# Performance work log

Measured on AMD Instinct MI355X. Metric: run time of the kernel, lower is better.

Reference implementation:

```python
import jax, jax.numpy as jnp
import numpy as np

TOP_K_FRACTION = 0.1


def setup_inputs() -> dict:
    key = jax.random.key(0)
    k1, k2, k3 = jax.random.split(key, 3)
    B, H, S, D = 2, 12, 1024, 64
    q = jax.random.normal(k1, (B, H, S, D), dtype=jnp.float32)
    k = jax.random.normal(k2, (B, H, S, D), dtype=jnp.float32)
    v = jax.random.normal(k3, (B, H, S, D), dtype=jnp.float32)
    mask = jnp.zeros((B, 1, 1, S), dtype=jnp.float32)
    return {"q": q, "k": k, "v": v, "mask": mask}


def reference(q, k, v, mask):
    B, H, S, D = q.shape
    k_precise = max(1, int(S * TOP_K_FRACTION))
    # binary (sign) approximation of attention scores; detached like torch
    q_bin = jnp.sign(jax.lax.stop_gradient(q))
    k_bin = jnp.sign(jax.lax.stop_gradient(k))
    approx_scores = jnp.einsum('bhsd,bhtd->bhst', q_bin, k_bin) / D  # [B,H,S,S]
    _, topk_idx = jax.lax.top_k(approx_scores, k_precise)  # [B,H,S,kp]
    # gather top-k keys/values per query: [B,H,S,kp,D]
    k_gathered = jnp.take_along_axis(k[:, :, None, :, :], topk_idx[..., None], axis=3)
    v_gathered = jnp.take_along_axis(v[:, :, None, :, :], topk_idx[..., None], axis=3)
    scale = np.float32(1.0 / np.sqrt(D))
    precise_scores = jnp.einsum('bhsd,bhskd->bhsk', q, k_gathered) * scale
    # gather mask along key positions: mask [B,1,1,S] -> [B,H,S,kp]
    mask_gathered = jnp.take_along_axis(
        jnp.broadcast_to(mask, (B, H, S, S)), topk_idx, axis=-1)
    precise_scores = precise_scores + mask_gathered
    precise_probs = jax.nn.softmax(precise_scores, axis=-1)
    attn_output = jnp.einsum('bhsk,bhskd->bhsd', precise_probs, v_gathered)
    return attn_output
```

## Files before the change

kernel.cpp:

```cpp
#include <hip/hip_runtime.h>
#include <hip/hip_fp16.h>
#include <cstdint>

#define BB 2
#define HH 12
#define SS 1024
#define DD 64
#define KP 102
#define KPAD 104
#define QPB 4
#define PFD 4

typedef _Float16 half2v __attribute__((ext_vector_type(2)));
typedef _Float16 half8v __attribute__((ext_vector_type(8)));
typedef float    f32x4  __attribute__((ext_vector_type(4)));

template <int CTRL>
__device__ __forceinline__ float dpp_f(float x) {
    return __builtin_bit_cast(float,
        __builtin_amdgcn_update_dpp(0, __builtin_bit_cast(int, x), CTRL, 0xF, 0xF, false));
}
__device__ __forceinline__ float group8_sum(float x) {
    x += dpp_f<0xB1>(x);
    x += dpp_f<0x4E>(x);
    x += dpp_f<0x141>(x);
    return x;
}
__device__ __forceinline__ int mbcnt64(unsigned long long m) {
    return (int)__builtin_amdgcn_mbcnt_hi((unsigned)(m >> 32),
               __builtin_amdgcn_mbcnt_lo((unsigned)(m & 0xffffffffull), 0u));
}
__device__ __forceinline__ half2v shfl_xor_h2(half2v v, int m) {
    return __builtin_bit_cast(half2v, __shfl_xor(__builtin_bit_cast(int, v), m));
}

#define GLOAD4(dst, a) asm volatile("global_load_dwordx4 %0, %1, off" : "=v"(dst) : "v"(a))
#define GLOAD1(dst, a) asm volatile("global_load_dword %0, %1, off"  : "=v"(dst) : "v"(a))
#define WAITV(n) do { asm volatile("s_waitcnt vmcnt(" #n ")");            \
                      __builtin_amdgcn_sched_barrier(0); } while (0)

__global__ __launch_bounds__(256) void pack_kernel(
    const float* __restrict__ k, const float* __restrict__ v,
    unsigned long long* __restrict__ kbits, _Float16* __restrict__ kvh)
{
    int row  = (int)((blockIdx.x * 256 + threadIdx.x) >> 6);
    int lane = (int)(threadIdx.x & 63);
    if (row >= BB * HH * SS) return;
    float kv = k[(size_t)row * DD + lane];
    float vv = v[(size_t)row * DD + lane];
    unsigned long long km = __ballot(kv > 0.0f);
    kvh[(size_t)row * 128 + lane]      = (_Float16)kv;
    kvh[(size_t)row * 128 + 64 + lane] = (_Float16)vv;
    if (lane == 0) kbits[row] = km;
}

__global__ __launch_bounds__(256, 4) void battn_kernel(
    const float* __restrict__ q, const _Float16* __restrict__ kvh,
    const float* __restrict__ mask,
    const unsigned long long* __restrict__ kbits,
    float* __restrict__ out)
{
    const int tid  = (int)threadIdx.x;
    const int w    = tid >> 6;
    const int lane = tid & 63;
    const int query = (int)blockIdx.x * QPB + w;
    const int bh    = query >> 10;
    const int b     = bh / HH;

    __shared__ __align__(16) int sel2[QPB][8][20];

    const float qreg = q[(size_t)query * DD + lane];
    const unsigned long long qm = __ballot(qreg > 0.0f);

    const unsigned long long* kb = kbits + (size_t)bh * SS;
    int pbin[16];
    #pragma unroll
    for (int j = 0; j < 16; ++j)
        pbin[j] = (int)__popcll(qm ^ kb[j * 64 + lane]);

    #define COUNT_LE(P, OUTC)                                      \
        { int _c = 0;                                              \
          _Pragma("unroll")                                        \
          for (int j = 0; j < 16; ++j)                             \
              _c += (int)__popcll(__ballot(pbin[j] <= (P)));       \
          (OUTC) = _c; }
    int P = 27, c, clt;
    COUNT_LE(P, c);
    if (c >= KP) {
        COUNT_LE(P - 1, clt);
        while (clt >= KP) { c = clt; --P; COUNT_LE(P - 1, clt); }
    } else {
        do { clt = c; ++P; COUNT_LE(P, c); } while (c < KP);
    }
    const int binP = P;
    const int need = KP - clt;
    #undef COUNT_LE

    if (lane < KPAD - KP) {
        int s = KP + lane;
        sel2[w][s & 7][s >> 3] = 0;
    }
    int base = 0, tie_base = 0;
    #pragma unroll
    for (int j = 0; j < 16; ++j) {
        bool isGt  = pbin[j] < binP;
        bool isTie = (pbin[j] == binP);
        unsigned long long tiem = __ballot(isTie);
        int rank = tie_base + mbcnt64(tiem);
        bool take = isGt || (isTie && rank < need);
        unsigned long long tm = __ballot(take);
        if (take) {
            int s = base + mbcnt64(tm);
            sel2[w][s & 7][s >> 3] = j * 64 + lane;
        }
        base     += (int)__popcll(tm);
        tie_base += (int)__popcll(tiem);
    }

    const int sub = lane & 7, g = lane >> 3;

    const float* qrow = q + (size_t)query * DD + sub * 8;
    half2v qh[4];
    #pragma unroll
    for (int d = 0; d < 4; ++d) {
        float2 f2 = *(const float2*)(qrow + d * 2);
        half2v h; h[0] = (_Float16)(f2.x * 0.125f); h[1] = (_Float16)(f2.y * 0.125f);
        qh[d] = h;
    }
    #pragma unroll
    for (int d = 0; d < 4; ++d) asm volatile("" : "+v"(qh[d]));

    const int* sp = &sel2[w][g][0];
    int tloc[13];
    {
        int4 t0 = *(const int4*)(sp);
        int4 t1 = *(const int4*)(sp + 4);
        int4 t2 = *(const int4*)(sp + 8);
        tloc[0] = t0.x; tloc[1]  = t0.y; tloc[2]  = t0.z; tloc[3]  = t0.w;
        tloc[4] = t1.x; tloc[5]  = t1.y; tloc[6]  = t1.z; tloc[7]  = t1.w;
        tloc[8] = t2.x; tloc[9]  = t2.y; tloc[10] = t2.z; tloc[11] = t2.w;
        tloc[12] = sp[12];
    }

    const _Float16* kvrows  = kvh + (size_t)bh * SS * 128;
    const uint64_t kvbase   = (uint64_t)((const char*)kvrows + sub * 16);
    const uint64_t maskbase = (uint64_t)(mask + (size_t)b * SS);

    f32x4 kreg[PFD], vreg[PFD];
    float mreg[PFD];

#define ISSUE(r, slot) do {                                               \
        const int _t = tloc[(r)];                                         \
        const uint64_t _ak = kvbase + (uint64_t)((unsigned)_t << 8);      \
        GLOAD4(kreg[(slot)], _ak);                                        \
        GLOAD4(vreg[(slot)], _ak + 128u);                                 \
        GLOAD1(mreg[(slot)], maskbase + (uint64_t)((unsigned)_t << 2));   \
    } while (0)

    half2v acch[4];
    #pragma unroll
    for (int d = 0; d < 4; ++d) { acch[d][0] = (_Float16)0; acch[d][1] = (_Float16)0; }
    float l_part = 0.0f;

#define CONSUME(ii, slot) do {                                            \
        half8v kv8 = __builtin_bit_cast(half8v, kreg[(slot)]);            \
        half8v vv8 = __builtin_bit_cast(half8v, vreg[(slot)]);            \
        float  mv  = mreg[(slot)];                                        \
        half2v k0; k0[0] = kv8[0]; k0[1] = kv8[1];                        \
        half2v k1; k1[0] = kv8[2]; k1[1] = kv8[3];                        \
        half2v k2; k2[0] = kv8[4]; k2[1] = kv8[5];                        \
        half2v k3; k3[0] = kv8[6]; k3[1] = kv8[7];                        \
        float s = fmaf(mv, 0.125f, -0.5f);                                \
        s = __builtin_amdgcn_fdot2(qh[0], k0, s, false);                  \
        s = __builtin_amdgcn_fdot2(qh[1], k1, s, false);                  \
        s = __builtin_amdgcn_fdot2(qh[2], k2, s, false);                  \
        s = __builtin_amdgcn_fdot2(qh[3], k3, s, false);                  \
        s = group8_sum(s);                                                \
        float e = __expf(s);                                              \
        if ((ii) == 12 && g >= (KP - 96)) e = 0.0f;                       \
        l_part += e;                                                      \
        _Float16 eh = (_Float16)e;                                        \
        half2v e2; e2[0] = eh; e2[1] = eh;                                \
        _Pragma("unroll")                                                 \
        for (int d = 0; d < 4; ++d) {                                     \
            half2v v2; v2[0] = vv8[d * 2]; v2[1] = vv8[d * 2 + 1];        \
            acch[d] = e2 * v2 + acch[d];                                  \
        }                                                                 \
    } while (0)

    ISSUE(0, 0); ISSUE(1, 1); ISSUE(2, 2); ISSUE(3, 3);

    WAITV(9); CONSUME(0, 0); ISSUE(4, 0);
    WAITV(9); CONSUME(1, 1); ISSUE(5, 1);
    WAITV(9); CONSUME(2, 2); ISSUE(6, 2);
    WAITV(9); CONSUME(3, 3); ISSUE(7, 3);
    WAITV(9); CONSUME(4, 0); ISSUE(8, 0);
    WAITV(9); CONSUME(5, 1); ISSUE(9, 1);
    WAITV(9); CONSUME(6, 2); ISSUE(10, 2);
    WAITV(9); CONSUME(7, 3); ISSUE(11, 3);
    WAITV(9); CONSUME(8, 0); ISSUE(12, 0);
    WAITV(9); CONSUME(9, 1);
    WAITV(6); CONSUME(10, 2);
    WAITV(3); CONSUME(11, 3);
    WAITV(0); CONSUME(12, 0);

#undef ISSUE
#undef CONSUME

    float l = l_part;
    l += __shfl_xor(l, 8);
    l += __shfl_xor(l, 16);
    l += __shfl_xor(l, 32);
    #pragma unroll
    for (int d = 0; d < 4; ++d) {
        acch[d] = acch[d] + shfl_xor_h2(acch[d], 8);
        acch[d] = acch[d] + shfl_xor_h2(acch[d], 16);
        acch[d] = acch[d] + shfl_xor_h2(acch[d], 32);
    }
    if (lane < 8) {
        const float rinv = __frcp_rn(l);
        float* orow = out + (size_t)query * DD + lane * 8;
        float4 o0 = make_float4((float)acch[0][0] * rinv, (float)acch[0][1] * rinv,
                                (float)acch[1][0] * rinv, (float)acch[1][1] * rinv);
        float4 o1 = make_float4((float)acch[2][0] * rinv, (float)acch[2][1] * rinv,
                                (float)acch[3][0] * rinv, (float)acch[3][1] * rinv);
        *(float4*)orow       = o0;
        *(float4*)(orow + 4) = o1;
    }
}

extern "C" void kernel_launch(void* const* d_in, const int* in_sizes, int n_in,
                              void* d_out, int out_size, void* d_ws, size_t ws_size,
                              hipStream_t stream) {
    const float* q    = (const float*)d_in[0];
    const float* k    = (const float*)d_in[1];
    const float* v    = (const float*)d_in[2];
    const float* mask = (const float*)d_in[3];
    float* out = (float*)d_out;

    const int rows = BB * HH * SS;
    unsigned long long* kbits = (unsigned long long*)d_ws;
    _Float16* kvh = (_Float16*)((char*)d_ws + (size_t)rows * sizeof(unsigned long long));

    pack_kernel<<<(rows * 64 + 255) / 256, 256, 0, stream>>>(k, v, kbits, kvh);
    battn_kernel<<<rows / QPB, 256, 0, stream>>>(q, kvh, mask, kbits, out);
}
```

Before: 110.8 us.

## Split fused top-k selection and gather-attention into separate kernels

Splits the single attention kernel in two. The first runs the popcount-based top-k selection and writes the chosen key indices as 16-bit values into a global workspace buffer. The second reads those indices and does the fp16 gather, softmax and weighted sum. The likely aim is to give each phase its own register and occupancy profile and drop the LDS staging, at the cost of an extra launch and a global round-trip for the indices.

```diff
diff --git a/kernel.cpp b/kernel.cpp
--- a/kernel.cpp
+++ b/kernel.cpp
@@ -10,6 +10,7 @@
 #define KPAD 104
 #define QPB 4
 #define PFD 4
+#define SELSTRIDE 104
 
 typedef _Float16 half2v __attribute__((ext_vector_type(2)));
 typedef _Float16 half8v __attribute__((ext_vector_type(8)));
@@ -54,20 +55,16 @@
     if (lane == 0) kbits[row] = km;
 }
 
-__global__ __launch_bounds__(256, 4) void battn_kernel(
-    const float* __restrict__ q, const _Float16* __restrict__ kvh,
-    const float* __restrict__ mask,
+__global__ __launch_bounds__(256, 4) void select_kernel(
+    const float* __restrict__ q,
     const unsigned long long* __restrict__ kbits,
-    float* __restrict__ out)
+    unsigned short* __restrict__ sel)
 {
     const int tid  = (int)threadIdx.x;
     const int w    = tid >> 6;
     const int lane = tid & 63;
     const int query = (int)blockIdx.x * QPB + w;
     const int bh    = query >> 10;
-    const int b     = bh / HH;
-
-    __shared__ __align__(16) int sel2[QPB][8][20];
 
     const float qreg = q[(size_t)query * DD + lane];
     const unsigned long long qm = __ballot(qreg > 0.0f);
@@ -96,10 +93,9 @@
     const int need = KP - clt;
     #undef COUNT_LE
 
-    if (lane < KPAD - KP) {
-        int s = KP + lane;
-        sel2[w][s & 7][s >> 3] = 0;
-    }
+    unsigned short* selq = sel + (size_t)query * SELSTRIDE;
+    if (lane < KPAD - KP)
+        selq[KP + lane] = 0;
     int base = 0, tie_base = 0;
     #pragma unroll
     for (int j = 0; j < 16; ++j) {
@@ -109,15 +105,31 @@
         int rank = tie_base + mbcnt64(tiem);
         bool take = isGt || (isTie && rank < need);
         unsigned long long tm = __ballot(take);
-        if (take) {
-            int s = base + mbcnt64(tm);
-            sel2[w][s & 7][s >> 3] = j * 64 + lane;
-        }
+        if (take)
+            selq[base + mbcnt64(tm)] = (unsigned short)(j * 64 + lane);
         base     += (int)__popcll(tm);
         tie_base += (int)__popcll(tiem);
     }
-
+}
+
+__global__ __launch_bounds__(256, 4) void gather_kernel(
+    const float* __restrict__ q, const _Float16* __restrict__ kvh,
+    const float* __restrict__ mask,
+    const unsigned short* __restrict__ sel,
+    float* __restrict__ out)
+{
+    const int tid  = (int)threadIdx.x;
+    const int w    = tid >> 6;
+    const int lane = tid & 63;
+    const int query = (int)blockIdx.x * QPB + w;
+    const int bh    = query >> 10;
+    const int b     = bh / HH;
     const int sub = lane & 7, g = lane >> 3;
+
+    const unsigned short* selg = sel + (size_t)query * SELSTRIDE + g;
+    int tloc[13];
+    #pragma unroll
+    for (int r = 0; r < 13; ++r) tloc[r] = (int)selg[r * 8];
 
     const float* qrow = q + (size_t)query * DD + sub * 8;
     half2v qh[4];
@@ -129,18 +141,8 @@
     }
     #pragma unroll
     for (int d = 0; d < 4; ++d) asm volatile("" : "+v"(qh[d]));
-
-    const int* sp = &sel2[w][g][0];
-    int tloc[13];
-    {
-        int4 t0 = *(const int4*)(sp);
-        int4 t1 = *(const int4*)(sp + 4);
-        int4 t2 = *(const int4*)(sp + 8);
-        tloc[0] = t0.x; tloc[1]  = t0.y; tloc[2]  = t0.z; tloc[3]  = t0.w;
-        tloc[4] = t1.x; tloc[5]  = t1.y; tloc[6]  = t1.z; tloc[7]  = t1.w;
-        tloc[8] = t2.x; tloc[9]  = t2.y; tloc[10] = t2.z; tloc[11] = t2.w;
-        tloc[12] = sp[12];
-    }
+    #pragma unroll
+    for (int r = 0; r < 13; ++r) asm volatile("" : "+v"(tloc[r]));
 
     const _Float16* kvrows  = kvh + (size_t)bh * SS * 128;
     const uint64_t kvbase   = (uint64_t)((const char*)kvrows + sub * 16);
@@ -239,9 +241,13 @@
     float* out = (float*)d_out;
 
     const int rows = BB * HH * SS;
-    unsigned long long* kbits = (unsigned long long*)d_ws;
-    _Float16* kvh = (_Float16*)((char*)d_ws + (size_t)rows * sizeof(unsigned long long));
+    char* ws = (char*)d_ws;
+    unsigned long long* kbits = (unsigned long long*)ws;
+    _Float16* kvh = (_Float16*)(ws + (size_t)rows * 8);
+    unsigned short* sel = (unsigned short*)(ws + (size_t)rows * 8
+                                               + (size_t)rows * 256);
 
     pack_kernel<<<(rows * 64 + 255) / 256, 256, 0, stream>>>(k, v, kbits, kvh);
-    battn_kernel<<<rows / QPB, 256, 0, stream>>>(q, kvh, mask, kbits, out);
-}
+    select_kernel<<<rows / QPB, 256, 0, stream>>>(q, kbits, sel);
+    gather_kernel<<<rows / QPB, 256, 0, stream>>>(q, kvh, mask, sel, out);
+}
```

Result: slower. 118.3 us (+6.8%).
